# Optimization experiments

Measured on AMD Instinct MI355X. Metric: run time of the kernel, lower is better.

Reference implementation:

```python
import jax, jax.numpy as jnp
import numpy as np

B, N, M, C = 4, 4096, 4096, 256
IMG_W, IMG_H = 1280.0, 384.0


def setup_inputs() -> dict:
    key = jax.random.key(0)
    ks = jax.random.split(key, 12)
    nodes_L = jax.random.normal(ks[0], (B, N, C), dtype=jnp.float32)
    nodes_R = jax.random.normal(ks[1], (B, M, C), dtype=jnp.float32)
    # pixel coordinates: (u, v) with u in [0, IMG_W), v in [0, IMG_H)
    scale = jnp.array([IMG_W, IMG_H], dtype=jnp.float32)
    kpts_L = jax.random.uniform(ks[2], (B, N, 2), dtype=jnp.float32) * scale
    kpts_R = jax.random.uniform(ks[3], (B, M, 2), dtype=jnp.float32) * scale
    s = 1.0 / np.sqrt(C)
    Wq = jax.random.normal(ks[4], (C, C), dtype=jnp.float32) * s
    bq = jnp.zeros((C,), dtype=jnp.float32)
    Wk = jax.random.normal(ks[5], (C, C), dtype=jnp.float32) * s
    bk = jnp.zeros((C,), dtype=jnp.float32)
    Wv = jax.random.normal(ks[6], (C, C), dtype=jnp.float32) * s
    bv = jnp.zeros((C,), dtype=jnp.float32)
    Wm = jax.random.normal(ks[7], (C, C), dtype=jnp.float32) * s
    bm = jnp.zeros((C,), dtype=jnp.float32)
    return {"nodes_L": nodes_L, "nodes_R": nodes_R, "kpts_L": kpts_L, "kpts_R": kpts_R,
            "Wq": Wq, "bq": bq, "Wk": Wk, "bk": bk, "Wv": Wv, "bv": bv, "Wm": Wm, "bm": bm}


def reference(nodes_L, nodes_R, kpts_L, kpts_R, Wq, bq, Wk, bk, Wv, bv, Wm, bm):
    dim = nodes_L.shape[-1]
    # torch Linear: x @ W.T + b
    Q = nodes_L @ Wq.T + bq                      # [B,N,C]
    K = nodes_R @ Wk.T + bk                      # [B,M,C]
    V = nodes_R @ Wv.T + bv                      # [B,M,C]
    # epipolar geometry terms, [B,N,M]
    dist_v = jnp.abs(kpts_L[:, :, 1:2] - kpts_R[:, :, 1][:, None, :])
    dist_u = kpts_L[:, :, 0:1] - kpts_R[:, :, 0][:, None, :]
    mask = (dist_v < 3.0) & (dist_u > 0) & (dist_u < 192)
    attn = jnp.einsum('bnc,bmc->bnm', Q, K) / jnp.sqrt(jnp.float32(dim))
    attn = jnp.where(mask, attn, jnp.float32(-1e9))
    attn_weights = jax.nn.softmax(attn, axis=-1)  # [B,N,M]
    matched = jnp.einsum('bnm,bmc->bnc', attn_weights, V)
    init_disparity = jnp.sum(attn_weights * dist_u, axis=-1, keepdims=True)  # [B,N,1]
    confidence = jnp.any(mask, axis=-1, keepdims=True).astype(jnp.float32)   # [B,N,1]
    return matched @ Wm.T + bm, init_disparity, confidence
```

## Files before the change

kernel.cpp:

```cpp
#include <hip/hip_runtime.h>
#include <hip/hip_bf16.h>

#define BB 4
#define NN 4096
#define MM 4096
#define CC 256
#define CAP 128
#define NBIN 384
#define NCH 16
#define CHK 256

typedef __attribute__((ext_vector_type(8))) short bf16x8;
typedef __attribute__((ext_vector_type(4))) float f32x4;

static __device__ __forceinline__ float bf2f(unsigned short u) {
    return __uint_as_float(((unsigned)u) << 16);
}
static __device__ __forceinline__ unsigned short f2bf(float f) {
    unsigned u = __float_as_uint(f);
    u += 0x7fffu + ((u >> 16) & 1u);
    return (unsigned short)(u >> 16);
}
static __device__ __forceinline__ bf16x8 asbf(uint4 u) {
    union { uint4 a; bf16x8 b; } c; c.a = u; return c.b;
}
static __device__ __forceinline__ void gload16(const unsigned short* g, unsigned short* l) {
    __builtin_amdgcn_global_load_lds(
        (const __attribute__((address_space(1))) unsigned int*)g,
        (__attribute__((address_space(3))) unsigned int*)l, 16, 0, 0);
}

__global__ __launch_bounds__(256) void prep_kernel(
    const float* __restrict__ Wq, const float* __restrict__ Wk,
    const float* __restrict__ Wv, const float* __restrict__ Wm,
    const float* __restrict__ L, const float* __restrict__ R,
    const float* __restrict__ kptsR,
    unsigned short* __restrict__ Wpk, unsigned short* __restrict__ Lpk,
    unsigned short* __restrict__ Rpk,
    int* __restrict__ hist, unsigned short* __restrict__ prank,
    float* __restrict__ Vsum, float* __restrict__ Usum)
{
    __shared__ __align__(16) unsigned char SMEM[32768];
    const int tid = threadIdx.x, y = blockIdx.y, x = blockIdx.x;

    if (y < 4) {
        const float* S = (y == 0) ? Wq : (y == 1) ? Wk : (y == 2) ? Wv : Wm;
        int o = x * 256 + tid;
        int j = o & 7, lane = (o >> 3) & 63, kt = o >> 9;
        int kk = kt >> 4, t = kt & 15;
        int r = t * 16 + (lane & 15), c = kk * 32 + (lane >> 4) * 8 + j;
        Wpk[(size_t)y * 65536 + o] = f2bf(S[r * 256 + c]);
        return;
    }
    if (y < 6) {
        const float* S = (y == 5) ? R : L;
        unsigned short* D = (y == 5) ? Rpk : Lpk;
        unsigned short* T = (unsigned short*)SMEM;
        const int wid = tid >> 6, lane = tid & 63;
        const size_t R0 = (size_t)x * 64;
#pragma unroll
        for (int it = 0; it < 16; ++it) {
            int row = it * 4 + wid;
            float4 f = *(const float4*)(S + (R0 + row) * 256 + lane * 4);
            ushort4 h = make_ushort4(f2bf(f.x), f2bf(f.y), f2bf(f.z), f2bf(f.w));
            int col = lane * 4;
            *(ushort4*)&T[row * 256 + (col ^ ((row & 7) << 3))] = h;
        }
        __syncthreads();
        unsigned short* Dp = D + (size_t)x * 16384;
#pragma unroll
        for (int p = 0; p < 8; ++p) {
            int u = p * 2048 + tid * 8;
            int rt = u >> 12, rem = u & 4095;
            int kk = rem >> 9, ln = (rem >> 3) & 63;
            int row = rt * 16 + (ln & 15);
            int col = kk * 32 + (ln >> 4) * 8;
            *(uint4*)(Dp + u) = *(const uint4*)&T[row * 256 + (col ^ ((row & 7) << 3))];
        }
        return;
    }
    if (y == 6) {
        if (x >= NCH * BB) return;
        int chunk = x & 15, b = x >> 4;
        int* h = (int*)SMEM;
        short* sbin = (short*)(SMEM + NBIN * 4);
        for (int i = tid; i < NBIN; i += CHK) h[i] = 0;
        int m = chunk * CHK + tid;
        float2 p = ((const float2*)kptsR)[(size_t)b * MM + m];
        int bin = (int)p.y;
        sbin[tid] = (short)bin;
        __syncthreads();
        atomicAdd(&h[bin], 1);
        int r = 0;
        for (int t = 0; t < tid; ++t) r += (sbin[t] == bin);
        prank[(b << 12) + m] = (unsigned short)r;
        __syncthreads();
        for (int i = tid; i < NBIN; i += CHK)
            hist[((size_t)b * NCH + chunk) * NBIN + i] = h[i];
        return;
    }
    if (x < BB) {
        int b = x;
        float s = 0.f;
        for (int m = tid; m < MM; m += 256) s += kptsR[((size_t)b * MM + m) * 2 + 0];
#pragma unroll
        for (int off = 32; off; off >>= 1) s += __shfl_xor(s, off);
        float* sr = (float*)SMEM;
        int wave = tid >> 6, lane = tid & 63;
        if (lane == 0) sr[wave] = s;
        __syncthreads();
        if (tid == 0) Usum[b] = sr[0] + sr[1] + sr[2] + sr[3];
    } else if (x == BB) {
        for (int i = tid; i < BB * CC; i += 256) Vsum[i] = 0.f;
    }
}

template <bool OUT_BF16>
__global__ __launch_bounds__(256, 4) void proj_mfma_kernel(
    const unsigned short* __restrict__ A0, const unsigned short* __restrict__ A1,
    const unsigned short* __restrict__ A2, const unsigned short* __restrict__ Wpk,
    const float* __restrict__ b0, const float* __restrict__ b1, const float* __restrict__ b2,
    void* __restrict__ O0, void* __restrict__ O1, void* __restrict__ O2,
    float* __restrict__ Vsum,
    const int* __restrict__ hist, int* __restrict__ binStart, int* __restrict__ chunkOff)
{
    __shared__ __align__(16) unsigned char SMEM[32768];
    const int tid = threadIdx.x, wid = tid >> 6, lane = tid & 63;
    const int y = blockIdx.y;

    if (y == 3) {
        if (blockIdx.x >= BB) return;
        int b = blockIdx.x;
        int* sc = (int*)SMEM;
        for (int v = tid; v < NBIN; v += 256) {
            int tot = 0;
            for (int c = 0; c < NCH; ++c) tot += hist[((size_t)b * NCH + c) * NBIN + v];
            sc[v] = tot;
        }
        __syncthreads();
        for (int off = 1; off < NBIN; off <<= 1) {
            int v1 = tid + 256;
            int t0 = (tid >= off) ? sc[tid - off] : 0;
            int t1 = (v1 < NBIN && v1 >= off) ? sc[v1 - off] : 0;
            __syncthreads();
            sc[tid] += t0;
            if (v1 < NBIN) sc[v1] += t1;
            __syncthreads();
        }
        for (int v = tid; v < NBIN; v += 256) {
            int start = v ? sc[v - 1] : 0;
            binStart[b * (NBIN + 1) + v] = start;
            if (v == NBIN - 1) binStart[b * (NBIN + 1) + NBIN] = sc[NBIN - 1];
            int run = start;
            for (int c = 0; c < NCH; ++c) {
                chunkOff[((size_t)b * NCH + c) * NBIN + v] = run;
                run += hist[((size_t)b * NCH + c) * NBIN + v];
            }
        }
        return;
    }

    const int lrow = lane & 15, lk = lane >> 4;
    const unsigned short* A = (y == 0) ? A0 : (y == 1) ? A1 : A2;
    const float* bias = (y == 0) ? b0 : (y == 1) ? b1 : b2;
    void* Out = (y == 0) ? O0 : (y == 1) ? O1 : O2;
    const unsigned short* W = Wpk + (size_t)y * 65536;

    const int bid = blockIdx.x;
    const int g = (bid >> 3) & 3;
    const int rblk = (bid & 7) + ((bid >> 5) << 3);
    const size_t rbase = (size_t)rblk * 128;
    const int rt0 = rblk * 8 + wid * 2;

    unsigned short* Wl = (unsigned short*)SMEM;
#pragma unroll
    for (int i = 0; i < 8; ++i) {
        int kk = wid * 2 + (i >> 2), q = i & 3;
        gload16(W + (size_t)kk * 8192 + g * 2048 + q * 512 + lane * 8,
                Wl + kk * 2048 + q * 512 + lane * 8);
    }

    const unsigned short* Ap = A + (size_t)rt0 * 4096 + lane * 8;
    uint4 a[2][2];
    a[0][0] = *(const uint4*)(Ap);
    a[0][1] = *(const uint4*)(Ap + 4096);

    f32x4 acc[4][2];
#pragma unroll
    for (int t = 0; t < 4; ++t) {
        acc[t][0] = (f32x4){0.f, 0.f, 0.f, 0.f};
        acc[t][1] = (f32x4){0.f, 0.f, 0.f, 0.f};
    }

    asm volatile("s_waitcnt vmcnt(0)" ::: "memory");
    __syncthreads();

#pragma unroll
    for (int kk = 0; kk < 8; ++kk) {
        const int cur = kk & 1, nxt = cur ^ 1;
        if (kk < 7) {
            a[nxt][0] = *(const uint4*)(Ap + (kk + 1) * 512);
            a[nxt][1] = *(const uint4*)(Ap + 4096 + (kk + 1) * 512);
        }
        bf16x8 af0 = asbf(a[cur][0]);
        bf16x8 af1 = asbf(a[cur][1]);
#pragma unroll
        for (int t = 0; t < 4; ++t) {
            bf16x8 wf = *(const bf16x8*)(Wl + kk * 2048 + t * 512 + lane * 8);
            acc[t][0] = __builtin_amdgcn_mfma_f32_16x16x32_bf16(af0, wf, acc[t][0], 0, 0, 0);
            acc[t][1] = __builtin_amdgcn_mfma_f32_16x16x32_bf16(af1, wf, acc[t][1], 0, 0, 0);
        }
    }

    if (Vsum != nullptr && y == 2) {
#pragma unroll
        for (int t = 0; t < 4; ++t) {
            int col = g * 64 + t * 16 + lrow;
            float vs = acc[t][0][0] + acc[t][0][1] + acc[t][0][2] + acc[t][0][3]
                     + acc[t][1][0] + acc[t][1][1] + acc[t][1][2] + acc[t][1][3];
            vs += __shfl_xor(vs, 16);
            vs += __shfl_xor(vs, 32);
            if (lk == 0)
                atomicAdd(&Vsum[(rblk >> 5) * CC + col], vs + 32.f * bias[col]);
        }
    }

    __syncthreads();
    if constexpr (OUT_BF16) {
        unsigned short* Bo = (unsigned short*)SMEM;
#pragma unroll
        for (int t = 0; t < 4; ++t) {
            float bb = bias[g * 64 + t * 16 + lrow];
#pragma unroll
            for (int s = 0; s < 2; ++s)
#pragma unroll
                for (int rr = 0; rr < 4; ++rr) {
                    int row = wid * 32 + s * 16 + lk * 4 + rr;
                    Bo[row * 64 + t * 16 + lrow] = f2bf(acc[t][s][rr] + bb);
                }
        }
        __syncthreads();
        unsigned short* O = (unsigned short*)Out;
#pragma unroll
        for (int it = 0; it < 4; ++it) {
            int idx = it * 2048 + tid * 8;
            int row = idx >> 6, col = idx & 63;
            *(uint4*)(O + (rbase + row) * CC + g * 64 + col) = *(const uint4*)&Bo[idx];
        }
    } else {
        float* Bo = (float*)SMEM;
#pragma unroll
        for (int t = 0; t < 4; ++t) {
            float bb = bias[g * 64 + t * 16 + lrow];
#pragma unroll
            for (int s = 0; s < 2; ++s)
#pragma unroll
                for (int rr = 0; rr < 4; ++rr) {
                    int row = wid * 32 + s * 16 + lk * 4 + rr;
                    Bo[row * 64 + t * 16 + lrow] = acc[t][s][rr] + bb;
                }
        }
        __syncthreads();
        float* O = (float*)Out;
#pragma unroll
        for (int it = 0; it < 8; ++it) {
            int idx = it * 1024 + tid * 4;
            int row = idx >> 6, col = idx & 63;
            *(float4*)(O + (rbase + row) * CC + g * 64 + col) = *(const float4*)&Bo[idx];
        }
    }
}

__global__ __launch_bounds__(256) void bin_place_kernel(
    const float* __restrict__ kptsR, const int* __restrict__ chunkOff,
    const unsigned short* __restrict__ prank,
    unsigned short* __restrict__ sortedM, float2* __restrict__ sortedUV)
{
    int tid = threadIdx.x, chunk = blockIdx.x, b = blockIdx.y;
    int m = chunk * CHK + tid;
    float2 p = ((const float2*)kptsR)[(size_t)b * MM + m];
    int bin = (int)p.y;
    int pos = chunkOff[((size_t)b * NCH + chunk) * NBIN + bin] + prank[(b << 12) + m];
    sortedM[(b << 12) + pos] = (unsigned short)m;
    sortedUV[(b << 12) + pos] = p;
}

static __device__ __forceinline__ size_t mt_po(int bn, int lane) {
    return ((size_t)(bn >> 4)) * 4096 + (size_t)(lane >> 3) * 512
         + (size_t)(((lane >> 1) & 3) * 16 + (bn & 15)) * 8 + (lane & 1) * 4;
}

__global__ __launch_bounds__(256) void attn_kernel(
    const unsigned short* __restrict__ Q, const unsigned short* __restrict__ K,
    const unsigned short* __restrict__ V,
    const float* __restrict__ kptsL,
    const int* __restrict__ binStart, const unsigned short* __restrict__ sortedM,
    const float2* __restrict__ sortedUV,
    const float* __restrict__ Vsum, const float* __restrict__ Usum,
    unsigned short* __restrict__ Mpk, float* __restrict__ out1, float* __restrict__ out2)
{
    __shared__ unsigned short s_m[4][CAP];
    __shared__ float s_du[4][CAP];
    __shared__ float s_p[4][CAP];

    const int wid = threadIdx.x >> 6, lane = threadIdx.x & 63;
    const int bn = blockIdx.x * 4 + wid;
    const int b = bn >> 12;

    float2 kl = *(const float2*)(kptsL + (size_t)bn * 2);
    float uL = kl.x, vL = kl.y;

    int ifl = (int)vL;
    int v0 = max(0, ifl - 3), v1 = min(NBIN - 1, ifl + 3);
    int s = binStart[b * (NBIN + 1) + v0];
    int e = binStart[b * (NBIN + 1) + v1 + 1];

    int cnt = 0;
    for (int i0 = s; i0 < e; i0 += 64) {
        int i = i0 + lane;
        bool valid = false;
        float du = 0.f;
        int m = 0;
        if (i < e) {
            float2 uv = sortedUV[(b << 12) + i];
            m = sortedM[(b << 12) + i];
            du = uL - uv.x;
            float dv = fabsf(vL - uv.y);
            valid = (dv < 3.0f) && (du > 0.0f) && (du < 192.0f);
        }
        unsigned long long bal = __ballot(valid);
        int pos = cnt + __popcll(bal & ((1ull << lane) - 1ull));
        if (valid && pos < CAP) { s_m[wid][pos] = (unsigned short)m; s_du[wid][pos] = du; }
        cnt += __popcll(bal);
    }
    if (cnt > CAP) cnt = CAP;

    if (cnt == 0) {
        float4 vs = *(const float4*)(Vsum + b * CC + lane * 4);
        ushort4 o = make_ushort4(f2bf(vs.x * (1.f / MM)), f2bf(vs.y * (1.f / MM)),
                                 f2bf(vs.z * (1.f / MM)), f2bf(vs.w * (1.f / MM)));
        *(ushort4*)(Mpk + mt_po(bn, lane)) = o;
        if (lane == 0) { out1[bn] = uL - Usum[b] * (1.f / MM); out2[bn] = 0.f; }
        return;
    }

    const int gi = lane >> 4, c = lane & 15;
    float qf[16];
    {
        const unsigned short* Qr = Q + (size_t)bn * CC + c * 16;
#pragma unroll
        for (int j = 0; j < 4; ++j) {
            ushort4 t = *(const ushort4*)(Qr + j * 4);
            qf[j * 4 + 0] = bf2f(t.x); qf[j * 4 + 1] = bf2f(t.y);
            qf[j * 4 + 2] = bf2f(t.z); qf[j * 4 + 3] = bf2f(t.w);
        }
    }
    const unsigned short* Kb = K + (((size_t)b) << 12) * CC;
    for (int i0 = 0; i0 < cnt; i0 += 4) {
        int i = i0 + gi;
        int m = s_m[wid][(i < cnt) ? i : 0];
        const unsigned short* Kr = Kb + (size_t)m * CC + c * 16;
        float d = 0.f;
#pragma unroll
        for (int j = 0; j < 4; ++j) {
            ushort4 t = *(const ushort4*)(Kr + j * 4);
            d += qf[j * 4 + 0] * bf2f(t.x) + qf[j * 4 + 1] * bf2f(t.y)
               + qf[j * 4 + 2] * bf2f(t.z) + qf[j * 4 + 3] * bf2f(t.w);
        }
        d += __shfl_xor(d, 8); d += __shfl_xor(d, 4);
        d += __shfl_xor(d, 2); d += __shfl_xor(d, 1);
        if (c == 0 && i < cnt) s_p[wid][i] = d;
    }

    const float NEG = -3.0e38f;
    float x0 = (lane < cnt) ? s_p[wid][lane] * 0.0625f : NEG;
    float x1 = (lane + 64 < cnt) ? s_p[wid][lane + 64] * 0.0625f : NEG;
    float mx = fmaxf(x0, x1);
#pragma unroll
    for (int off = 32; off; off >>= 1) mx = fmaxf(mx, __shfl_xor(mx, off));
    float p0 = (lane < cnt) ? expf(x0 - mx) : 0.f;
    float p1 = (lane + 64 < cnt) ? expf(x1 - mx) : 0.f;
    float d0 = (lane < cnt) ? s_du[wid][lane] : 0.f;
    float d1 = (lane + 64 < cnt) ? s_du[wid][lane + 64] : 0.f;
    float ps = p0 + p1, ds = p0 * d0 + p1 * d1;
#pragma unroll
    for (int off = 32; off; off >>= 1) { ps += __shfl_xor(ps, off); ds += __shfl_xor(ds, off); }
    float inv = 1.f / ps;
    if (lane < cnt) s_p[wid][lane] = p0 * inv;
    if (lane + 64 < cnt) s_p[wid][lane + 64] = p1 * inv;

    const unsigned short* Vb = V + (((size_t)b) << 12) * CC;
    float a0 = 0.f, a1 = 0.f, a2 = 0.f, a3 = 0.f;
    float e0 = 0.f, e1 = 0.f, e2 = 0.f, e3 = 0.f;
    int i = 0;
    for (; i + 1 < cnt; i += 2) {
        float w0 = s_p[wid][i], w1 = s_p[wid][i + 1];
        ushort4 va = *(const ushort4*)(Vb + (size_t)s_m[wid][i] * CC + lane * 4);
        ushort4 vb = *(const ushort4*)(Vb + (size_t)s_m[wid][i + 1] * CC + lane * 4);
        a0 += w0 * bf2f(va.x); a1 += w0 * bf2f(va.y);
        a2 += w0 * bf2f(va.z); a3 += w0 * bf2f(va.w);
        e0 += w1 * bf2f(vb.x); e1 += w1 * bf2f(vb.y);
        e2 += w1 * bf2f(vb.z); e3 += w1 * bf2f(vb.w);
    }
    if (i < cnt) {
        float w0 = s_p[wid][i];
        ushort4 va = *(const ushort4*)(Vb + (size_t)s_m[wid][i] * CC + lane * 4);
        a0 += w0 * bf2f(va.x); a1 += w0 * bf2f(va.y);
        a2 += w0 * bf2f(va.z); a3 += w0 * bf2f(va.w);
    }
    ushort4 o = make_ushort4(f2bf(a0 + e0), f2bf(a1 + e1), f2bf(a2 + e2), f2bf(a3 + e3));
    *(ushort4*)(Mpk + mt_po(bn, lane)) = o;
    if (lane == 0) { out1[bn] = ds * inv; out2[bn] = 1.f; }
}

extern "C" void kernel_launch(void* const* d_in, const int* in_sizes, int n_in,
                              void* d_out, int out_size, void* d_ws, size_t ws_size,
                              hipStream_t stream) {
    const float* nodes_L = (const float*)d_in[0];
    const float* nodes_R = (const float*)d_in[1];
    const float* kpts_L  = (const float*)d_in[2];
    const float* kpts_R  = (const float*)d_in[3];
    const float* Wq = (const float*)d_in[4];
    const float* bq = (const float*)d_in[5];
    const float* Wk = (const float*)d_in[6];
    const float* bk = (const float*)d_in[7];
    const float* Wv = (const float*)d_in[8];
    const float* bv = (const float*)d_in[9];
    const float* Wm = (const float*)d_in[10];
    const float* bm = (const float*)d_in[11];

    char* ws = (char*)d_ws;
    unsigned short* Wpk = (unsigned short*)ws; ws += (size_t)4 * 65536 * 2;
    unsigned short* Lpk = (unsigned short*)ws; ws += (size_t)BB * NN * CC * 2;
    unsigned short* Rpk = (unsigned short*)ws; ws += (size_t)BB * MM * CC * 2;
    unsigned short* Qp  = (unsigned short*)ws; ws += (size_t)BB * NN * CC * 2;
    unsigned short* Kp  = (unsigned short*)ws; ws += (size_t)BB * MM * CC * 2;
    unsigned short* Vp  = (unsigned short*)ws; ws += (size_t)BB * MM * CC * 2;
    unsigned short* Mpk = (unsigned short*)ws; ws += (size_t)BB * NN * CC * 2;
    float* Vsum = (float*)ws;        ws += (size_t)BB * CC * 4;
    float* Usum = (float*)ws;        ws += (size_t)BB * 4;
    float2* sortedUV = (float2*)ws;  ws += (size_t)BB * MM * 8;
    int* binStart = (int*)ws;        ws += (size_t)BB * (NBIN + 1) * 4;
    unsigned short* sortedM = (unsigned short*)ws; ws += (size_t)BB * MM * 2;
    int* hist = (int*)ws;            ws += (size_t)BB * NCH * NBIN * 4;
    int* chunkOff = (int*)ws;        ws += (size_t)BB * NCH * NBIN * 4;
    unsigned short* prank = (unsigned short*)ws;

    float* out0 = (float*)d_out;
    float* out1 = out0 + (size_t)BB * NN * CC;
    float* out2 = out1 + (size_t)BB * NN;

    prep_kernel<<<dim3(256, 8), dim3(256), 0, stream>>>(
        Wq, Wk, Wv, Wm, nodes_L, nodes_R, kpts_R,
        Wpk, Lpk, Rpk, hist, prank, Vsum, Usum);

    proj_mfma_kernel<true><<<dim3(512, 4), dim3(256), 0, stream>>>(
        Lpk, Rpk, Rpk, Wpk, bq, bk, bv, Qp, Kp, Vp, Vsum,
        hist, binStart, chunkOff);

    bin_place_kernel<<<dim3(NCH, BB), dim3(256), 0, stream>>>(
        kpts_R, chunkOff, prank, sortedM, sortedUV);

    attn_kernel<<<dim3(BB * NN / 4), dim3(256), 0, stream>>>(
        Qp, Kp, Vp, kpts_L, binStart, sortedM, sortedUV, Vsum, Usum, Mpk, out1, out2);

    proj_mfma_kernel<false><<<dim3(512, 1), dim3(256), 0, stream>>>(
        Mpk, nullptr, nullptr, Wpk + 3 * 65536, bm, nullptr, nullptr,
        out0, nullptr, nullptr, nullptr, nullptr, nullptr, nullptr);
}
```

Measured before the change: 66.43 us.

## Fold bin placement into scan blocks, hoist Q load, specialize small-count softmax

Moves the bin-placement scatter into the y==3 scan blocks of the projection kernel. Each block caches the histogram in shared memory and walks the chunks with running exclusive offsets, so the separate launch and the chunkOff buffer go away. The attention kernel now loads Q before the candidate gather so that load latency overlaps, and it uses a single-register softmax path when there are at most 64 candidates. The trade-off is serialized per-chunk scatter with syncs inside 4 blocks, and Q loads are now issued even for rows with no candidates.

Result: slower. 69.95 us (+5.3%).

```diff
diff --git a/kernel.cpp b/kernel.cpp
--- a/kernel.cpp
+++ b/kernel.cpp
@@ -122,7 +122,9 @@
     const float* __restrict__ b0, const float* __restrict__ b1, const float* __restrict__ b2,
     void* __restrict__ O0, void* __restrict__ O1, void* __restrict__ O2,
     float* __restrict__ Vsum,
-    const int* __restrict__ hist, int* __restrict__ binStart, int* __restrict__ chunkOff)
+    const int* __restrict__ hist, int* __restrict__ binStart,
+    const float* __restrict__ kptsR, const unsigned short* __restrict__ prank,
+    unsigned short* __restrict__ sortedM, float2* __restrict__ sortedUV)
 {
     __shared__ __align__(16) unsigned char SMEM[32768];
     const int tid = threadIdx.x, wid = tid >> 6, lane = tid & 63;
@@ -130,32 +132,45 @@
 
     if (y == 3) {
         if (blockIdx.x >= BB) return;
-        int b = blockIdx.x;
-        int* sc = (int*)SMEM;
+        const int b = blockIdx.x;
+        int* h2  = (int*)SMEM;
+        int* inc = (int*)(SMEM + 24576);
+        int* ex  = (int*)(SMEM + 26112);
+        for (int i = tid; i < NCH * NBIN; i += 256)
+            h2[i] = hist[(size_t)b * NCH * NBIN + i];
+        __syncthreads();
         for (int v = tid; v < NBIN; v += 256) {
             int tot = 0;
-            for (int c = 0; c < NCH; ++c) tot += hist[((size_t)b * NCH + c) * NBIN + v];
-            sc[v] = tot;
+#pragma unroll
+            for (int c = 0; c < NCH; ++c) tot += h2[c * NBIN + v];
+            inc[v] = tot;
         }
         __syncthreads();
         for (int off = 1; off < NBIN; off <<= 1) {
             int v1 = tid + 256;
-            int t0 = (tid >= off) ? sc[tid - off] : 0;
-            int t1 = (v1 < NBIN && v1 >= off) ? sc[v1 - off] : 0;
+            int t0 = (tid >= off) ? inc[tid - off] : 0;
+            int t1 = (v1 < NBIN && v1 >= off) ? inc[v1 - off] : 0;
             __syncthreads();
-            sc[tid] += t0;
-            if (v1 < NBIN) sc[v1] += t1;
+            inc[tid] += t0;
+            if (v1 < NBIN) inc[v1] += t1;
             __syncthreads();
         }
         for (int v = tid; v < NBIN; v += 256) {
-            int start = v ? sc[v - 1] : 0;
-            binStart[b * (NBIN + 1) + v] = start;
-            if (v == NBIN - 1) binStart[b * (NBIN + 1) + NBIN] = sc[NBIN - 1];
-            int run = start;
-            for (int c = 0; c < NCH; ++c) {
-                chunkOff[((size_t)b * NCH + c) * NBIN + v] = run;
-                run += hist[((size_t)b * NCH + c) * NBIN + v];
-            }
+            binStart[b * (NBIN + 1) + v] = v ? inc[v - 1] : 0;
+            ex[v] = v ? inc[v - 1] : 0;
+        }
+        if (tid == 0) binStart[b * (NBIN + 1) + NBIN] = inc[NBIN - 1];
+        __syncthreads();
+        for (int c = 0; c < NCH; ++c) {
+            int m = c * CHK + tid;
+            float2 p = ((const float2*)kptsR)[(size_t)b * MM + m];
+            int bin = (int)p.y;
+            int pos = ex[bin] + prank[(b << 12) + m];
+            sortedM[(b << 12) + pos] = (unsigned short)m;
+            sortedUV[(b << 12) + pos] = p;
+            __syncthreads();
+            for (int v = tid; v < NBIN; v += 256) ex[v] += h2[c * NBIN + v];
+            __syncthreads();
         }
         return;
     }
@@ -269,20 +284,6 @@
             *(float4*)(O + (rbase + row) * CC + g * 64 + col) = *(const float4*)&Bo[idx];
         }
     }
-}
-
-__global__ __launch_bounds__(256) void bin_place_kernel(
-    const float* __restrict__ kptsR, const int* __restrict__ chunkOff,
-    const unsigned short* __restrict__ prank,
-    unsigned short* __restrict__ sortedM, float2* __restrict__ sortedUV)
-{
-    int tid = threadIdx.x, chunk = blockIdx.x, b = blockIdx.y;
-    int m = chunk * CHK + tid;
-    float2 p = ((const float2*)kptsR)[(size_t)b * MM + m];
-    int bin = (int)p.y;
-    int pos = chunkOff[((size_t)b * NCH + chunk) * NBIN + bin] + prank[(b << 12) + m];
-    sortedM[(b << 12) + pos] = (unsigned short)m;
-    sortedUV[(b << 12) + pos] = p;
 }
 
 static __device__ __forceinline__ size_t mt_po(int bn, int lane) {
@@ -307,6 +308,18 @@
     const int bn = blockIdx.x * 4 + wid;
     const int b = bn >> 12;
 
+    const int gi = lane >> 4, c = lane & 15;
+    float qf[16];
+    {
+        const unsigned short* Qr = Q + (size_t)bn * CC + c * 16;
+#pragma unroll
+        for (int j = 0; j < 4; ++j) {
+            ushort4 t = *(const ushort4*)(Qr + j * 4);
+            qf[j * 4 + 0] = bf2f(t.x); qf[j * 4 + 1] = bf2f(t.y);
+            qf[j * 4 + 2] = bf2f(t.z); qf[j * 4 + 3] = bf2f(t.w);
+        }
+    }
+
     float2 kl = *(const float2*)(kptsL + (size_t)bn * 2);
     float uL = kl.x, vL = kl.y;
 
@@ -344,17 +357,6 @@
         return;
     }
 
-    const int gi = lane >> 4, c = lane & 15;
-    float qf[16];
-    {
-        const unsigned short* Qr = Q + (size_t)bn * CC + c * 16;
-#pragma unroll
-        for (int j = 0; j < 4; ++j) {
-            ushort4 t = *(const ushort4*)(Qr + j * 4);
-            qf[j * 4 + 0] = bf2f(t.x); qf[j * 4 + 1] = bf2f(t.y);
-            qf[j * 4 + 2] = bf2f(t.z); qf[j * 4 + 3] = bf2f(t.w);
-        }
-    }
     const unsigned short* Kb = K + (((size_t)b) << 12) * CC;
     for (int i0 = 0; i0 < cnt; i0 += 4) {
         int i = i0 + gi;
@@ -373,21 +375,36 @@
     }
 
     const float NEG = -3.0e38f;
-    float x0 = (lane < cnt) ? s_p[wid][lane] * 0.0625f : NEG;
-    float x1 = (lane + 64 < cnt) ? s_p[wid][lane + 64] * 0.0625f : NEG;
-    float mx = fmaxf(x0, x1);
-#pragma unroll
-    for (int off = 32; off; off >>= 1) mx = fmaxf(mx, __shfl_xor(mx, off));
-    float p0 = (lane < cnt) ? expf(x0 - mx) : 0.f;
-    float p1 = (lane + 64 < cnt) ? expf(x1 - mx) : 0.f;
-    float d0 = (lane < cnt) ? s_du[wid][lane] : 0.f;
-    float d1 = (lane + 64 < cnt) ? s_du[wid][lane + 64] : 0.f;
-    float ps = p0 + p1, ds = p0 * d0 + p1 * d1;
-#pragma unroll
-    for (int off = 32; off; off >>= 1) { ps += __shfl_xor(ps, off); ds += __shfl_xor(ds, off); }
-    float inv = 1.f / ps;
-    if (lane < cnt) s_p[wid][lane] = p0 * inv;
-    if (lane + 64 < cnt) s_p[wid][lane + 64] = p1 * inv;
+    float mx, ps, ds, inv;
+    if (cnt <= 64) {
+        float x0 = (lane < cnt) ? s_p[wid][lane] * 0.0625f : NEG;
+        mx = x0;
+#pragma unroll
+        for (int off = 32; off; off >>= 1) mx = fmaxf(mx, __shfl_xor(mx, off));
+        float p0 = (lane < cnt) ? expf(x0 - mx) : 0.f;
+        float d0 = (lane < cnt) ? s_du[wid][lane] : 0.f;
+        ps = p0; ds = p0 * d0;
+#pragma unroll
+        for (int off = 32; off; off >>= 1) { ps += __shfl_xor(ps, off); ds += __shfl_xor(ds, off); }
+        inv = 1.f / ps;
+        if (lane < cnt) s_p[wid][lane] = p0 * inv;
+    } else {
+        float x0 = (lane < cnt) ? s_p[wid][lane] * 0.0625f : NEG;
+        float x1 = (lane + 64 < cnt) ? s_p[wid][lane + 64] * 0.0625f : NEG;
+        mx = fmaxf(x0, x1);
+#pragma unroll
+        for (int off = 32; off; off >>= 1) mx = fmaxf(mx, __shfl_xor(mx, off));
+        float p0 = (lane < cnt) ? expf(x0 - mx) : 0.f;
+        float p1 = (lane + 64 < cnt) ? expf(x1 - mx) : 0.f;
+        float d0 = (lane < cnt) ? s_du[wid][lane] : 0.f;
+        float d1 = (lane + 64 < cnt) ? s_du[wid][lane + 64] : 0.f;
+        ps = p0 + p1; ds = p0 * d0 + p1 * d1;
+#pragma unroll
+        for (int off = 32; off; off >>= 1) { ps += __shfl_xor(ps, off); ds += __shfl_xor(ds, off); }
+        inv = 1.f / ps;
+        if (lane < cnt) s_p[wid][lane] = p0 * inv;
+        if (lane + 64 < cnt) s_p[wid][lane + 64] = p1 * inv;
+    }
 
     const unsigned short* Vb = V + (((size_t)b) << 12) * CC;
     float a0 = 0.f, a1 = 0.f, a2 = 0.f, a3 = 0.f;
@@ -443,7 +460,6 @@
     int* binStart = (int*)ws;        ws += (size_t)BB * (NBIN + 1) * 4;
     unsigned short* sortedM = (unsigned short*)ws; ws += (size_t)BB * MM * 2;
     int* hist = (int*)ws;            ws += (size_t)BB * NCH * NBIN * 4;
-    int* chunkOff = (int*)ws;        ws += (size_t)BB * NCH * NBIN * 4;
     unsigned short* prank = (unsigned short*)ws;
 
     float* out0 = (float*)d_out;
@@ -456,15 +472,13 @@
 
     proj_mfma_kernel<true><<<dim3(512, 4), dim3(256), 0, stream>>>(
         Lpk, Rpk, Rpk, Wpk, bq, bk, bv, Qp, Kp, Vp, Vsum,
-        hist, binStart, chunkOff);
-
-    bin_place_kernel<<<dim3(NCH, BB), dim3(256), 0, stream>>>(
-        kpts_R, chunkOff, prank, sortedM, sortedUV);
+        hist, binStart, kpts_R, prank, sortedM, sortedUV);
 
     attn_kernel<<<dim3(BB * NN / 4), dim3(256), 0, stream>>>(
         Qp, Kp, Vp, kpts_L, binStart, sortedM, sortedUV, Vsum, Usum, Mpk, out1, out2);
 
     proj_mfma_kernel<false><<<dim3(512, 1), dim3(256), 0, stream>>>(
         Mpk, nullptr, nullptr, Wpk + 3 * 65536, bm, nullptr, nullptr,
-        out0, nullptr, nullptr, nullptr, nullptr, nullptr, nullptr);
-}
+        out0, nullptr, nullptr, nullptr,
+        nullptr, nullptr, nullptr, nullptr, nullptr, nullptr);
+}
```
